# Kernel optimization log

Hardware: AMD Instinct MI355X
Metric: run time of the kernel (lower is better)

The kernel has to match this reference:

```python
import math
import jax, jax.numpy as jnp
import numpy as np

SIZE = 1.0            # scene cube extent; positions live in [-SIZE/2, SIZE/2]
N_LEVELS = 16         # number of hash-grid resolutions
TABLE_SIZE = 524288   # 2**19 entries per level
FEAT_DIM = 2          # features per entry
N_POINTS = 262144     # query points (rays * samples)
BASE_RES, MAX_RES = 16, 512

_PRIMES = jnp.array([1, 2654435761, 805459861], dtype=jnp.uint32)
# 8 corner offsets of a voxel, [8,3]
_OFFS = jnp.array([[(c >> 2) & 1, (c >> 1) & 1, c & 1] for c in range(8)], dtype=jnp.uint32)


def _level_lookup(xyz01, table, res):
    # xyz01: [N,3] in [0,1); table: [T,F]; res: scalar int32
    x = xyz01 * res.astype(xyz01.dtype)          # [N,3] grid coords
    x0f = jnp.floor(x)
    w = x - x0f                                  # [N,3] trilinear fracs
    x0 = x0f.astype(jnp.uint32)
    corners = x0[:, None, :] + _OFFS[None]       # [N,8,3]
    h = corners * _PRIMES                        # uint32 wraparound multiply
    idx = (h[..., 0] ^ h[..., 1] ^ h[..., 2]) % jnp.uint32(TABLE_SIZE)  # [N,8]
    feats = table[idx]                           # [N,8,F] gather
    ws = jnp.prod(jnp.where(_OFFS[None] == 1, w[:, None, :], 1.0 - w[:, None, :]), axis=-1)  # [N,8]
    return jnp.einsum('nc,ncf->nf', ws, feats)   # [N,F]


def _forward(xyz, tables, resolutions):
    # xyz: [N,3] in scene coords; tables: [L,T,F]; resolutions: [L] int32
    xyz01 = jnp.clip(xyz / SIZE + 0.5, 0.0, 1.0 - 1e-6)
    per_level = jax.vmap(_level_lookup, in_axes=(None, 0, 0))(xyz01, tables, resolutions)  # [L,N,F]
    return jnp.transpose(per_level, (1, 0, 2)).reshape(xyz.shape[0], N_LEVELS * FEAT_DIM)


def setup_inputs() -> dict:
    key = jax.random.key(0)
    k1, k2 = jax.random.split(key)
    xyz = (jax.random.uniform(k1, (N_POINTS, 3), dtype=jnp.float32) - 0.5) * SIZE
    tables = jax.random.normal(k2, (N_LEVELS, TABLE_SIZE, FEAT_DIM), dtype=jnp.float32) * 1e-2
    growth = (MAX_RES / BASE_RES) ** (1.0 / (N_LEVELS - 1))
    res = np.round(BASE_RES * growth ** np.arange(N_LEVELS)).astype(np.int32)
    return {"xyz": xyz, "tables": tables, "resolutions": jnp.array(res)}


def reference(xyz, tables, resolutions):
    return _forward(xyz, tables, resolutions)
```

## Files before the change

kernel.cpp:

```cpp
#include <hip/hip_runtime.h>


#define HG_N_LEVELS   16
#define HG_TABLE_SIZE 524288u
#define HG_TABLE_MASK (HG_TABLE_SIZE - 1u)

typedef float vf2 __attribute__((ext_vector_type(2)));
typedef float vf4 __attribute__((ext_vector_type(4)));

__device__ __forceinline__ void hg_prep2(
    float px, float py, float pz, float res,
    unsigned* __restrict__ s, float* __restrict__ wyz,
    unsigned* __restrict__ x0out, float* __restrict__ wx)
{
    const float lim = 1.0f - 1e-6f;
    float ux = fminf(fmaxf(px + 0.5f, 0.0f), lim);
    float uy = fminf(fmaxf(py + 0.5f, 0.0f), lim);
    float uz = fminf(fmaxf(pz + 0.5f, 0.0f), lim);
    float fx = ux * res, fy = uy * res, fz = uz * res;
    float x0f = floorf(fx), y0f = floorf(fy), z0f = floorf(fz);
    float wx1 = fx - x0f, wy1 = fy - y0f, wz1 = fz - z0f;
    float wx0 = 1.0f - wx1, wy0 = 1.0f - wy1, wz0 = 1.0f - wz1;
    unsigned x0 = (unsigned)x0f, y0 = (unsigned)y0f, z0 = (unsigned)z0f;
    const unsigned P1 = 2654435761u, P2 = 805459861u;
    unsigned hy0 = y0 * P1, hy1 = (y0 + 1u) * P1;
    unsigned hz0 = z0 * P2, hz1 = (z0 + 1u) * P2;
    s[0] = hy0 ^ hz0;  wyz[0] = wy0 * wz0;
    s[1] = hy0 ^ hz1;  wyz[1] = wy0 * wz1;
    s[2] = hy1 ^ hz0;  wyz[2] = wy1 * wz0;
    s[3] = hy1 ^ hz1;  wyz[3] = wy1 * wz1;
    *x0out = x0; wx[0] = wx0; wx[1] = wx1;
}

__device__ __forceinline__ void hg_prep(
    float px, float py, float pz, float res,
    unsigned* __restrict__ idx, float* __restrict__ w)
{
    unsigned s[4]; float wyz[4], wx[2]; unsigned x0;
    hg_prep2(px, py, pz, res, s, wyz, &x0, wx);
    #pragma unroll
    for (int j = 0; j < 4; ++j) {
        idx[j]     = (x0 ^ s[j]) & HG_TABLE_MASK;        w[j]     = wx[0] * wyz[j];
        idx[4 + j] = ((x0 + 1u) ^ s[j]) & HG_TABLE_MASK; w[4 + j] = wx[1] * wyz[j];
    }
}

__device__ __forceinline__ vf4 hg_gather2(
    const float2* __restrict__ tbl, float res,
    float ax, float ay, float az, float bx, float by, float bz)
{
    unsigned sA[4], sB[4], x0A, x0B;
    float wyzA[4], wyzB[4], wxA[2], wxB[2];
    hg_prep2(ax, ay, az, res, sA, wyzA, &x0A, wxA);
    hg_prep2(bx, by, bz, res, sB, wyzB, &x0B, wxB);

    unsigned iA0[4], iA1[4], iB0[4], iB1[4];
    #pragma unroll
    for (int j = 0; j < 4; ++j) {
        iA0[j] = (x0A ^ sA[j]) & HG_TABLE_MASK;
        iA1[j] = ((x0A + 1u) ^ sA[j]) & HG_TABLE_MASK;
        iB0[j] = (x0B ^ sB[j]) & HG_TABLE_MASK;
        iB1[j] = ((x0B + 1u) ^ sB[j]) & HG_TABLE_MASK;
    }
    const bool oddA = (x0A & 1u) != 0u;
    const bool oddB = (x0B & 1u) != 0u;

    vf4 qA[4], qB[4];
    #pragma unroll
    for (int j = 0; j < 4; ++j) qA[j] = *(const vf4*)(tbl + (iA0[j] & ~1u));
    #pragma unroll
    for (int j = 0; j < 4; ++j) qB[j] = *(const vf4*)(tbl + (iB0[j] & ~1u));

    vf2 eA[4], eB[4];
    #pragma unroll
    for (int j = 0; j < 4; ++j) { eA[j] = (vf2)(0.f); eB[j] = (vf2)(0.f); }
    if (oddA) {
        #pragma unroll
        for (int j = 0; j < 4; ++j) eA[j] = *(const vf2*)(tbl + iA1[j]);
    }
    if (oddB) {
        #pragma unroll
        for (int j = 0; j < 4; ++j) eB[j] = *(const vf2*)(tbl + iB1[j]);
    }

    asm volatile(""
        : "+v"(qA[0]), "+v"(qA[1]), "+v"(qA[2]), "+v"(qA[3]),
          "+v"(qB[0]), "+v"(qB[1]), "+v"(qB[2]), "+v"(qB[3]),
          "+v"(eA[0]), "+v"(eA[1]), "+v"(eA[2]), "+v"(eA[3]),
          "+v"(eB[0]), "+v"(eB[1]), "+v"(eB[2]), "+v"(eB[3])
        :
        : "memory");

    float oax = 0.f, oay = 0.f, obx = 0.f, oby = 0.f;
    #pragma unroll
    for (int j = 0; j < 4; ++j) {
        bool hi = (iA0[j] & 1u) != 0u;
        vf2 lo;  lo.x  = qA[j].x; lo.y  = qA[j].y;
        vf2 hiv; hiv.x = qA[j].z; hiv.y = qA[j].w;
        vf2 f0 = hi ? hiv : lo;
        vf2 f1 = oddA ? eA[j] : (hi ? lo : hiv);
        float w0 = wxA[0] * wyzA[j], w1 = wxA[1] * wyzA[j];
        oax += w0 * f0.x + w1 * f1.x;
        oay += w0 * f0.y + w1 * f1.y;
    }
    #pragma unroll
    for (int j = 0; j < 4; ++j) {
        bool hi = (iB0[j] & 1u) != 0u;
        vf2 lo;  lo.x  = qB[j].x; lo.y  = qB[j].y;
        vf2 hiv; hiv.x = qB[j].z; hiv.y = qB[j].w;
        vf2 f0 = hi ? hiv : lo;
        vf2 f1 = oddB ? eB[j] : (hi ? lo : hiv);
        float w0 = wxB[0] * wyzB[j], w1 = wxB[1] * wyzB[j];
        obx += w0 * f0.x + w1 * f1.x;
        oby += w0 * f0.y + w1 * f1.y;
    }

    vf4 r; r.x = oax; r.y = oay; r.z = obx; r.w = oby;
    return r;
}

__device__ __forceinline__ vf2 hg_gather1(
    const float2* __restrict__ tbl, float res,
    float px, float py, float pz)
{
    unsigned idx[8]; float w[8];
    hg_prep(px, py, pz, res, idx, w);
    vf2 f[8];
    #pragma unroll
    for (int k = 0; k < 8; ++k) f[k] = *(const vf2*)(tbl + idx[k]);
    float sx = 0.f, sy = 0.f;
    #pragma unroll
    for (int k = 0; k < 8; ++k) { sx += w[k] * f[k].x; sy += w[k] * f[k].y; }
    vf2 v; v.x = sx; v.y = sy;
    return v;
}

__global__ __launch_bounds__(256) void hashgrid_pa(
    const float* __restrict__ xyz,
    const float* __restrict__ tables,
    const int*   __restrict__ resolutions,
    float*       __restrict__ ws,
    int n_points)
{
    const int x     = blockIdx.x & 7;
    const int chunk = blockIdx.x >> 3;
    const int level = 2 * x + 1;

    const float res = (float)resolutions[level];
    const float2* __restrict__ tbl =
        (const float2*)tables + (size_t)level * HG_TABLE_SIZE;
    float* __restrict__ wrow = ws + (size_t)x * n_points * 2;

    const int p0 = (chunk << 9) + ((int)threadIdx.x << 1);
    if (p0 >= n_points) return;

    if (p0 + 1 < n_points) {
        const float* xp = xyz + (size_t)p0 * 3;
        vf2 c0 = *(const vf2*)(xp);
        vf2 c1 = *(const vf2*)(xp + 2);
        vf2 c2 = *(const vf2*)(xp + 4);
        vf4 v = hg_gather2(tbl, res, c0.x, c0.y, c1.x, c1.y, c2.x, c2.y);
        __builtin_nontemporal_store(v, (vf4*)(wrow + 2 * (size_t)p0));
    } else {
        vf2 v = hg_gather1(tbl, res,
                           xyz[(size_t)p0 * 3 + 0],
                           xyz[(size_t)p0 * 3 + 1],
                           xyz[(size_t)p0 * 3 + 2]);
        __builtin_nontemporal_store(v, (vf2*)(wrow + 2 * (size_t)p0));
    }
}

__global__ __launch_bounds__(256) void hashgrid_pb(
    const float* __restrict__ xyz,
    const float* __restrict__ tables,
    const int*   __restrict__ resolutions,
    const float* __restrict__ ws,
    float*       __restrict__ out,
    int n_points)
{
    const int x     = blockIdx.x & 7;
    const int chunk = blockIdx.x >> 3;
    const int level = 2 * x;

    const float res = (float)resolutions[level];
    const float2* __restrict__ tbl =
        (const float2*)tables + (size_t)level * HG_TABLE_SIZE;
    const float* __restrict__ wrow = ws + (size_t)x * n_points * 2;

    const int p0 = (chunk << 9) + ((int)threadIdx.x << 1);
    if (p0 >= n_points) return;

    if (p0 + 1 < n_points) {
        vf4 wsv = __builtin_nontemporal_load((const vf4*)(wrow + 2 * (size_t)p0));
        asm volatile("" : "+v"(wsv));

        const float* xp = xyz + (size_t)p0 * 3;
        vf2 c0 = *(const vf2*)(xp);
        vf2 c1 = *(const vf2*)(xp + 2);
        vf2 c2 = *(const vf2*)(xp + 4);
        vf4 g = hg_gather2(tbl, res, c0.x, c0.y, c1.x, c1.y, c2.x, c2.y);

        vf4 o0; o0.x = g.x; o0.y = g.y; o0.z = wsv.x; o0.w = wsv.y;
        vf4 o1; o1.x = g.z; o1.y = g.w; o1.z = wsv.z; o1.w = wsv.w;
        float* op = out + (size_t)p0 * 32 + 4 * x;
        __builtin_nontemporal_store(o0, (vf4*)op);
        __builtin_nontemporal_store(o1, (vf4*)(op + 32));
    } else {
        vf2 wsv = __builtin_nontemporal_load((const vf2*)(wrow + 2 * (size_t)p0));
        vf2 g = hg_gather1(tbl, res,
                           xyz[(size_t)p0 * 3 + 0],
                           xyz[(size_t)p0 * 3 + 1],
                           xyz[(size_t)p0 * 3 + 2]);
        vf4 o; o.x = g.x; o.y = g.y; o.z = wsv.x; o.w = wsv.y;
        __builtin_nontemporal_store(o, (vf4*)(out + (size_t)p0 * 32 + 4 * x));
    }
}

__global__ __launch_bounds__(256) void hashgrid_fwd(
    const float* __restrict__ xyz,
    const float* __restrict__ tables,
    const int*   __restrict__ resolutions,
    float*       __restrict__ out,
    int n_points)
{
    int tid   = blockIdx.x * blockDim.x + threadIdx.x;
    int point = tid >> 4;
    int level = tid & 15;
    if (point >= n_points) return;

    float px = xyz[point * 3 + 0];
    float py = xyz[point * 3 + 1];
    float pz = xyz[point * 3 + 2];
    float res = (float)resolutions[level];
    const float2* __restrict__ tbl =
        (const float2*)tables + (size_t)level * HG_TABLE_SIZE;

    vf2 v = hg_gather1(tbl, res, px, py, pz);
    *(vf2*)(out + (size_t)point * 32 + 2 * level) = v;
}

extern "C" void kernel_launch(void* const* d_in, const int* in_sizes, int n_in,
                              void* d_out, int out_size, void* d_ws, size_t ws_size,
                              hipStream_t stream) {
    const float* xyz         = (const float*)d_in[0];
    const float* tables      = (const float*)d_in[1];
    const int*   resolutions = (const int*)d_in[2];
    float*       out         = (float*)d_out;

    int n_points = in_sizes[0] / 3;
    size_t ws_needed = (size_t)n_points * 8 * sizeof(float2);

    if (ws_size >= ws_needed) {
        float* ws = (float*)d_ws;
        int C = (n_points + 511) >> 9;
        hashgrid_pa<<<8 * C, 256, 0, stream>>>(
            xyz, tables, resolutions, ws, n_points);
        hashgrid_pb<<<8 * C, 256, 0, stream>>>(
            xyz, tables, resolutions, ws, out, n_points);
    } else {
        int n_threads = n_points * HG_N_LEVELS;
        hashgrid_fwd<<<(n_threads + 255) / 256, 256, 0, stream>>>(
            xyz, tables, resolutions, out, n_points);
    }
}
```

Baseline: 231.6 us.

## Fuse two-pass hash-grid kernels into one launch with level-ordered block schedule

Replaces the two-kernel scheme, which staged odd levels in a workspace and merged them in a second pass, with a single kernel that writes each level's features directly to the output as 8-byte stores. Blocks are ordered so the high-resolution levels 8-15 run first across all chunks, then level 7, then levels 0-6. This is meant to keep each table hot in L2 while it is in use and to remove the workspace round-trip and the second launch. In exchange, the output stores become narrower and strided per point.

After: 236.5 us. 1.02x slower.

```diff
diff --git a/kernel.cpp b/kernel.cpp
--- a/kernel.cpp
+++ b/kernel.cpp
@@ -135,108 +135,52 @@
     return v;
 }
 
-__global__ __launch_bounds__(256) void hashgrid_pa(
+__global__ __launch_bounds__(256) void hashgrid_fused(
     const float* __restrict__ xyz,
     const float* __restrict__ tables,
     const int*   __restrict__ resolutions,
-    float*       __restrict__ ws,
+    float*       __restrict__ out,
     int n_points)
 {
-    const int x     = blockIdx.x & 7;
-    const int chunk = blockIdx.x >> 3;
-    const int level = 2 * x + 1;
+    const int x    = blockIdx.x & 7;
+    const int slot = blockIdx.x >> 3;
+    const int C    = (n_points + 511) >> 9;
+    const int C8   = (C + 7) >> 3;
+
+    int level, chunk;
+    if (slot < C)            { level = 8 + x; chunk = slot; }
+    else if (slot < C + C8)  { int j = slot - C; level = 7; chunk = x + (j << 3); }
+    else                     { int j = slot - C - C8;
+                               if (x >= 6) { level = 6; chunk = (x - 6) + (j << 1); }
+                               else        { level = x; chunk = j; } }
+    if (chunk >= C) return;
 
     const float res = (float)resolutions[level];
     const float2* __restrict__ tbl =
         (const float2*)tables + (size_t)level * HG_TABLE_SIZE;
-    float* __restrict__ wrow = ws + (size_t)x * n_points * 2;
 
     const int p0 = (chunk << 9) + ((int)threadIdx.x << 1);
     if (p0 >= n_points) return;
+
+    float* op = out + (size_t)p0 * 32 + 2 * level;
 
     if (p0 + 1 < n_points) {
         const float* xp = xyz + (size_t)p0 * 3;
         vf2 c0 = *(const vf2*)(xp);
         vf2 c1 = *(const vf2*)(xp + 2);
         vf2 c2 = *(const vf2*)(xp + 4);
-        vf4 v = hg_gather2(tbl, res, c0.x, c0.y, c1.x, c1.y, c2.x, c2.y);
-        __builtin_nontemporal_store(v, (vf4*)(wrow + 2 * (size_t)p0));
+        vf4 g = hg_gather2(tbl, res, c0.x, c0.y, c1.x, c1.y, c2.x, c2.y);
+        vf2 a; a.x = g.x; a.y = g.y;
+        vf2 b; b.x = g.z; b.y = g.w;
+        __builtin_nontemporal_store(a, (vf2*)op);
+        __builtin_nontemporal_store(b, (vf2*)(op + 32));
     } else {
-        vf2 v = hg_gather1(tbl, res,
-                           xyz[(size_t)p0 * 3 + 0],
-                           xyz[(size_t)p0 * 3 + 1],
-                           xyz[(size_t)p0 * 3 + 2]);
-        __builtin_nontemporal_store(v, (vf2*)(wrow + 2 * (size_t)p0));
-    }
-}
-
-__global__ __launch_bounds__(256) void hashgrid_pb(
-    const float* __restrict__ xyz,
-    const float* __restrict__ tables,
-    const int*   __restrict__ resolutions,
-    const float* __restrict__ ws,
-    float*       __restrict__ out,
-    int n_points)
-{
-    const int x     = blockIdx.x & 7;
-    const int chunk = blockIdx.x >> 3;
-    const int level = 2 * x;
-
-    const float res = (float)resolutions[level];
-    const float2* __restrict__ tbl =
-        (const float2*)tables + (size_t)level * HG_TABLE_SIZE;
-    const float* __restrict__ wrow = ws + (size_t)x * n_points * 2;
-
-    const int p0 = (chunk << 9) + ((int)threadIdx.x << 1);
-    if (p0 >= n_points) return;
-
-    if (p0 + 1 < n_points) {
-        vf4 wsv = __builtin_nontemporal_load((const vf4*)(wrow + 2 * (size_t)p0));
-        asm volatile("" : "+v"(wsv));
-
-        const float* xp = xyz + (size_t)p0 * 3;
-        vf2 c0 = *(const vf2*)(xp);
-        vf2 c1 = *(const vf2*)(xp + 2);
-        vf2 c2 = *(const vf2*)(xp + 4);
-        vf4 g = hg_gather2(tbl, res, c0.x, c0.y, c1.x, c1.y, c2.x, c2.y);
-
-        vf4 o0; o0.x = g.x; o0.y = g.y; o0.z = wsv.x; o0.w = wsv.y;
-        vf4 o1; o1.x = g.z; o1.y = g.w; o1.z = wsv.z; o1.w = wsv.w;
-        float* op = out + (size_t)p0 * 32 + 4 * x;
-        __builtin_nontemporal_store(o0, (vf4*)op);
-        __builtin_nontemporal_store(o1, (vf4*)(op + 32));
-    } else {
-        vf2 wsv = __builtin_nontemporal_load((const vf2*)(wrow + 2 * (size_t)p0));
         vf2 g = hg_gather1(tbl, res,
                            xyz[(size_t)p0 * 3 + 0],
                            xyz[(size_t)p0 * 3 + 1],
                            xyz[(size_t)p0 * 3 + 2]);
-        vf4 o; o.x = g.x; o.y = g.y; o.z = wsv.x; o.w = wsv.y;
-        __builtin_nontemporal_store(o, (vf4*)(out + (size_t)p0 * 32 + 4 * x));
-    }
-}
-
-__global__ __launch_bounds__(256) void hashgrid_fwd(
-    const float* __restrict__ xyz,
-    const float* __restrict__ tables,
-    const int*   __restrict__ resolutions,
-    float*       __restrict__ out,
-    int n_points)
-{
-    int tid   = blockIdx.x * blockDim.x + threadIdx.x;
-    int point = tid >> 4;
-    int level = tid & 15;
-    if (point >= n_points) return;
-
-    float px = xyz[point * 3 + 0];
-    float py = xyz[point * 3 + 1];
-    float pz = xyz[point * 3 + 2];
-    float res = (float)resolutions[level];
-    const float2* __restrict__ tbl =
-        (const float2*)tables + (size_t)level * HG_TABLE_SIZE;
-
-    vf2 v = hg_gather1(tbl, res, px, py, pz);
-    *(vf2*)(out + (size_t)point * 32 + 2 * level) = v;
+        __builtin_nontemporal_store(g, (vf2*)op);
+    }
 }
 
 extern "C" void kernel_launch(void* const* d_in, const int* in_sizes, int n_in,
@@ -248,18 +192,9 @@
     float*       out         = (float*)d_out;
 
     int n_points = in_sizes[0] / 3;
-    size_t ws_needed = (size_t)n_points * 8 * sizeof(float2);
-
-    if (ws_size >= ws_needed) {
-        float* ws = (float*)d_ws;
-        int C = (n_points + 511) >> 9;
-        hashgrid_pa<<<8 * C, 256, 0, stream>>>(
-            xyz, tables, resolutions, ws, n_points);
-        hashgrid_pb<<<8 * C, 256, 0, stream>>>(
-            xyz, tables, resolutions, ws, out, n_points);
-    } else {
-        int n_threads = n_points * HG_N_LEVELS;
-        hashgrid_fwd<<<(n_threads + 255) / 256, 256, 0, stream>>>(
-            xyz, tables, resolutions, out, n_points);
-    }
-}
+    int C  = (n_points + 511) >> 9;
+    int C8 = (C + 7) >> 3;
+    int slots = 2 * C + C8;
+    hashgrid_fused<<<8 * slots, 256, 0, stream>>>(
+        xyz, tables, resolutions, out, n_points);
+}
```
